# Kernel optimization log

Hardware: AMD Instinct MI355X
Metric: run time of the kernel (lower is better)

Reference implementation:

```python
import jax, jax.numpy as jnp
import numpy as np

B, L, D0, H, K = 16, 256, 64, 128, 512  # batch, seq, feat, hidden, codebook size


def _p(key, shape, scale=0.05):
    return jax.random.normal(key, shape, jnp.float32) * scale


def setup_inputs() -> dict:
    key = jax.random.key(0)
    ks = jax.random.split(key, 32)
    inp = {
        "inputs": jax.random.normal(ks[0], (B, L, D0), jnp.float32),
        "input_lens": jnp.full((B,), L, dtype=jnp.int64),
        "in_mask": jnp.ones((B, L), jnp.float32),
        # encoder params
        "enc_lin1_W": _p(ks[1], (H, D0)), "enc_lin1_b": jnp.zeros((H,), jnp.float32),
        "enc_Wih_f": _p(ks[2], (4 * H, H)), "enc_Whh_f": _p(ks[3], (4 * H, H)), "enc_b_f": jnp.zeros((4 * H,), jnp.float32),
        "enc_Wih_b": _p(ks[4], (4 * H, H)), "enc_Whh_b": _p(ks[5], (4 * H, H)), "enc_b_b": jnp.zeros((4 * H,), jnp.float32),
        "enc_lin2_W": _p(ks[6], (H, 2 * H)), "enc_lin2_b": jnp.zeros((H,), jnp.float32),
        # VQ codebook (K codes of dim H), init uniform(-1/K, 1/K) as in torch
        "vq_emb": jax.random.uniform(ks[7], (K, H), jnp.float32, -1.0 / K, 1.0 / K),
        # decoder params
        "dec_lin1_W": _p(ks[8], (H, D0)), "dec_lin1_b": jnp.zeros((H,), jnp.float32),
        "dec_Wih": _p(ks[9], (4 * H, H)), "dec_Whh": _p(ks[10], (4 * H, H)), "dec_b": jnp.zeros((4 * H,), jnp.float32),
        "attn_Wq": _p(ks[11], (H, H)), "attn_bq": jnp.zeros((H,), jnp.float32),
        "attn_Wk": _p(ks[12], (H, H)), "attn_bk": jnp.zeros((H,), jnp.float32),
        "attn_Wv": _p(ks[13], (H, H)), "attn_bv": jnp.zeros((H,), jnp.float32),
        "dec_lin2_W": _p(ks[14], (D0, H)), "dec_lin2_b": jnp.zeros((D0,), jnp.float32),
    }
    return inp


def _lstm_cell(x, h, c, Wih, Whh, b):
    g = x @ Wih.T + h @ Whh.T + b  # (B, 4H)
    i, f, gg, o = jnp.split(g, 4, axis=-1)
    c = jax.nn.sigmoid(f) * c + jax.nn.sigmoid(i) * jnp.tanh(gg)
    h = jax.nn.sigmoid(o) * jnp.tanh(c)
    return h, c


def _lstm_scan(x_blh, Wih, Whh, b, reverse=False):
    Bb = x_blh.shape[0]
    Hh = Whh.shape[1]
    init = (jnp.zeros((Bb, Hh), x_blh.dtype), jnp.zeros((Bb, Hh), x_blh.dtype))

    def step(carry, x):
        h, c = _lstm_cell(x, carry[0], carry[1], Wih, Whh, b)
        return (h, c), h

    _, hs = jax.lax.scan(step, init, jnp.swapaxes(x_blh, 0, 1), reverse=reverse)
    return jnp.swapaxes(hs, 0, 1)  # (B, L, H)


def _forward(inputs, in_mask, p):
    # ---- encoder: Linear -> ReLU -> BiLSTM -> Linear (full-length sequences) ----
    enc_x = jax.nn.relu(inputs @ p["enc_lin1_W"].T + p["enc_lin1_b"])
    hf = _lstm_scan(enc_x, p["enc_Wih_f"], p["enc_Whh_f"], p["enc_b_f"], reverse=False)
    hb = _lstm_scan(enc_x, p["enc_Wih_b"], p["enc_Whh_b"], p["enc_b_b"], reverse=True)
    ze = jnp.concatenate([hf, hb], axis=-1) @ p["enc_lin2_W"].T + p["enc_lin2_b"]  # (B,L,H)

    # ---- VQ: nearest codebook entry (expanded ||a-b||^2, avoids (B,L,K,C) tensor) ----
    emb = p["vq_emb"]  # (K, H)
    dist = (jnp.sum(ze * ze, -1, keepdims=True)
            - 2.0 * jnp.einsum("blc,kc->blk", ze, emb)
            + jnp.sum(emb * emb, -1)[None, None, :])  # (B,L,K)
    nearest = jnp.argmin(dist, axis=-1)  # (B,L) int
    zq = emb[nearest]  # (B,L,H)
    dec_in = ze + jax.lax.stop_gradient(zq - ze)  # straight-through

    k_proj = dec_in @ p["attn_Wk"].T + p["attn_bk"]  # (B,L,H)
    v_proj = dec_in @ p["attn_Wv"].T + p["attn_bv"]
    scale = 1.0 / jnp.sqrt(jnp.float32(H))
    mask_add = jnp.where(in_mask == 0, -1e9, 0.0).astype(jnp.float32)  # (B,L)

    def dec_step(carry, _):
        h, c, tok = carry
        x = jax.nn.relu(tok @ p["dec_lin1_W"].T + p["dec_lin1_b"])  # (B,H)
        h, c = _lstm_cell(x, h, c, p["dec_Wih"], p["dec_Whh"], p["dec_b"])
        q = h @ p["attn_Wq"].T + p["attn_bq"]  # (B,H)
        scores = jnp.einsum("bd,bld->bl", q, k_proj) * scale + mask_add
        attn = jax.nn.softmax(scores, axis=-1)  # (B,L)
        ctx = jnp.einsum("bl,bld->bd", attn, v_proj)  # (B,H)
        out = ctx @ p["dec_lin2_W"].T + p["dec_lin2_b"]  # (B,D0)
        return (h, c, out), (out, attn)

    Bb = inputs.shape[0]
    init = (jnp.zeros((Bb, H), jnp.float32), jnp.zeros((Bb, H), jnp.float32), jnp.zeros((Bb, D0), jnp.float32))
    _, (outs, attns) = jax.lax.scan(dec_step, init, None, length=dec_in.shape[1])
    dec_out = jnp.swapaxes(outs, 0, 1)  # (B,L,D0)
    attn_w = jnp.swapaxes(attns, 0, 1)  # (B,L,L)
    return dec_out, attn_w, ze, zq


def reference(inputs, input_lens, in_mask, enc_lin1_W, enc_lin1_b, enc_Wih_f, enc_Whh_f, enc_b_f,
              enc_Wih_b, enc_Whh_b, enc_b_b, enc_lin2_W, enc_lin2_b, vq_emb,
              dec_lin1_W, dec_lin1_b, dec_Wih, dec_Whh, dec_b,
              attn_Wq, attn_bq, attn_Wk, attn_bk, attn_Wv, attn_bv, dec_lin2_W, dec_lin2_b):
    p = dict(enc_lin1_W=enc_lin1_W, enc_lin1_b=enc_lin1_b, enc_Wih_f=enc_Wih_f, enc_Whh_f=enc_Whh_f,
             enc_b_f=enc_b_f, enc_Wih_b=enc_Wih_b, enc_Whh_b=enc_Whh_b, enc_b_b=enc_b_b,
             enc_lin2_W=enc_lin2_W, enc_lin2_b=enc_lin2_b, vq_emb=vq_emb,
             dec_lin1_W=dec_lin1_W, dec_lin1_b=dec_lin1_b, dec_Wih=dec_Wih, dec_Whh=dec_Whh, dec_b=dec_b,
             attn_Wq=attn_Wq, attn_bq=attn_bq, attn_Wk=attn_Wk, attn_bk=attn_bk,
             attn_Wv=attn_Wv, attn_bv=attn_bv, dec_lin2_W=dec_lin2_W, dec_lin2_b=dec_lin2_b)
    return _forward(inputs, in_mask, p)
```

## Files before the change

### kernel.cpp

```cpp
#include <hip/hip_runtime.h>

#define Bn  16
#define Ln  256
#define D0n 64
#define Hn  128
#define H4n 512
#define Kn  512
#define BLn 4096

typedef float f4 __attribute__((ext_vector_type(4)));
typedef unsigned long long u64;

__device__ __forceinline__ float sigf(float x) { return 1.0f / (1.0f + expf(-x)); }

__device__ __forceinline__ float fma4v(f4 w, f4 x, float acc) {
    acc = fmaf(w.x, x.x, acc);
    acc = fmaf(w.y, x.y, acc);
    acc = fmaf(w.z, x.z, acc);
    acc = fmaf(w.w, x.w, acc);
    return acc;
}

__device__ __forceinline__ float dotn(const f4* __restrict__ a,
                                      const f4* __restrict__ w, int n4) {
    float a0 = 0.f, a1 = 0.f, a2 = 0.f, a3 = 0.f;
    for (int i = 0; i < n4; i += 4) {
        a0 = fma4v(a[i], w[i], a0);
        a1 = fma4v(a[i + 1], w[i + 1], a1);
        a2 = fma4v(a[i + 2], w[i + 2], a2);
        a3 = fma4v(a[i + 3], w[i + 3], a3);
    }
    return (a0 + a1) + (a2 + a3);
}

__device__ __forceinline__ void tag_store(u64* p, float v, unsigned tag) {
    u64 pk = ((u64)tag << 32) | (u64)__float_as_uint(v);
    __hip_atomic_store(p, pk, __ATOMIC_RELAXED, __HIP_MEMORY_SCOPE_AGENT);
}
__device__ __forceinline__ float tag_poll(u64* p, unsigned tag) {
    u64 v;
    do {
        v = __hip_atomic_load(p, __ATOMIC_RELAXED, __HIP_MEMORY_SCOPE_AGENT);
    } while ((unsigned)(v >> 32) != tag);
    return __uint_as_float((unsigned)v);
}

__global__ __launch_bounds__(256)
void k_gemm(const float* __restrict__ X, const float* __restrict__ W,
            const float* __restrict__ b, float* __restrict__ Y,
            int K, int out_dim, int do_relu, float scale) {
    __shared__ __align__(16) f4 wt4[4096];
    const int K4 = K >> 2;
    const int tid = threadIdx.x;
    const int c = tid & 63, rpart = tid >> 6;
    const f4* W4 = (const f4*)W;
    const int per = K4 >> 2;
    for (int j = 0; j < per; ++j) {
        int col = rpart * per + j;
        wt4[col * 64 + c] = W4[(size_t)(blockIdx.x * 64 + c) * K4 + col];
    }
    __syncthreads();
    const f4* X4 = (const f4*)X;
    const float bc = b ? b[blockIdx.x * 64 + c] : 0.f;
    const int cidx = blockIdx.x * 64 + c;
    for (int i = 0; i < 4; ++i) {
        int rbase = blockIdx.y * 64 + i * 16 + rpart * 4;
        const f4* xr0 = X4 + (size_t)(rbase + 0) * K4;
        const f4* xr1 = X4 + (size_t)(rbase + 1) * K4;
        const f4* xr2 = X4 + (size_t)(rbase + 2) * K4;
        const f4* xr3 = X4 + (size_t)(rbase + 3) * K4;
        float a0 = 0.f, a1 = 0.f, a2 = 0.f, a3 = 0.f;
        for (int k4 = 0; k4 < K4; ++k4) {
            f4 wv = wt4[k4 * 64 + c];
            a0 = fma4v(wv, xr0[k4], a0);
            a1 = fma4v(wv, xr1[k4], a1);
            a2 = fma4v(wv, xr2[k4], a2);
            a3 = fma4v(wv, xr3[k4], a3);
        }
        a0 = scale * a0 + bc; a1 = scale * a1 + bc;
        a2 = scale * a2 + bc; a3 = scale * a3 + bc;
        if (do_relu) {
            a0 = fmaxf(a0, 0.f); a1 = fmaxf(a1, 0.f);
            a2 = fmaxf(a2, 0.f); a3 = fmaxf(a3, 0.f);
        }
        Y[(size_t)(rbase + 0) * out_dim + cidx] = a0;
        Y[(size_t)(rbase + 1) * out_dim + cidx] = a1;
        Y[(size_t)(rbase + 2) * out_dim + cidx] = a2;
        Y[(size_t)(rbase + 3) * out_dim + cidx] = a3;
    }
}

__global__ void k_prep(const float* __restrict__ attn_Wq, float* __restrict__ WqT,
                       const f4* __restrict__ dec_Wih, f4* __restrict__ WihL,
                       const f4* __restrict__ whf, const f4* __restrict__ whb,
                       f4* __restrict__ WhhL, int* __restrict__ zbuf) {
    const int blk = blockIdx.x, tid = threadIdx.x;
    if (blk < 64) {
        int idx = blk * 256 + tid;
        int c = idx >> 7, r = idx & 127;
        WqT[idx] = attn_Wq[(size_t)r * Hn + c];
    } else if (blk < 128) {
        int idx = (blk - 64) * 256 + tid;
        int t = idx & 511, side = (idx >> 9) & 1, k = idx >> 10;
        int rl = t >> 1;
        int grow = (rl >> 6) * 128 + side * 64 + (rl & 63);
        WihL[idx] = dec_Wih[(size_t)grow * 32 + (t & 1) * 16 + k];
    } else if (blk < 192) {
        int idx = (blk - 128) * 256 + tid;
        int row = idx & 511, k = (idx >> 9) & 15, dir = idx >> 13;
        const f4* src = dir ? whb : whf;
        WhhL[idx] = src[(size_t)row * 32 + 16 + k];
    } else {
        int idx = (blk - 192) * 256 + tid;
        if (idx < 8192) zbuf[idx] = 0;
    }
}

__global__ void k_rearrKQF(const f4* __restrict__ in, f4* __restrict__ out) {
    int idx = blockIdx.x * blockDim.x + threadIdx.x;
    if (idx >= 131072) return;
    int tid = idx & 511, k = (idx >> 9) & 15, b = idx >> 13;
    out[idx] = in[((size_t)b * 256 + (tid >> 1)) * 32 + (tid & 1) * 16 + k];
}

__global__ void k_cst(const float* __restrict__ kp, const float* __restrict__ bq,
                      const float* __restrict__ mask, float* __restrict__ cst) {
    int p = blockIdx.x * blockDim.x + threadIdx.x;
    if (p >= BLn) return;
    float a = dotn((const f4*)bq, (const f4*)(kp + (size_t)p * Hn), Hn >> 2);
    cst[p] = a * 0.088388347648318447f + (mask[p] == 0.f ? -1e9f : 0.f);
}

__global__ void k_codenorm(const float* __restrict__ emb, float* __restrict__ c2) {
    int k = blockIdx.x * blockDim.x + threadIdx.x;
    if (k >= Kn) return;
    const f4* e4 = (const f4*)(emb + (size_t)k * Hn);
    float acc = 0.f;
    for (int i = 0; i < Hn / 4; ++i) {
        f4 v = e4[i];
        acc = fmaf(v.x, v.x, acc); acc = fmaf(v.y, v.y, acc);
        acc = fmaf(v.z, v.z, acc); acc = fmaf(v.w, v.w, acc);
    }
    c2[k] = acc;
}

__global__ __launch_bounds__(128)
void k_vqpick(const float* __restrict__ dist, const float* __restrict__ emb,
              float* __restrict__ zq) {
    const int p = blockIdx.x, tid = threadIdx.x;
    __shared__ int best_s;
    if (tid < 64) {
        float best = 3.0e38f; int bi = 0;
        for (int j = 0; j < 8; ++j) {
            int k = j * 64 + tid;
            float d = dist[(size_t)p * Kn + k];
            if (d < best) { best = d; bi = k; }
        }
        for (int off = 32; off > 0; off >>= 1) {
            float ov = __shfl_xor(best, off);
            int   oi = __shfl_xor(bi, off);
            if (ov < best || (ov == best && oi < bi)) { best = ov; bi = oi; }
        }
        if (tid == 0) best_s = bi;
    }
    __syncthreads();
    zq[(size_t)p * Hn + tid] = emb[(size_t)best_s * Hn + tid];
}

__global__ __launch_bounds__(512, 1)
void k_lstm3(const float* __restrict__ xWf, const float* __restrict__ xWb,
             const float* __restrict__ Whh_f, const float* __restrict__ Whh_b,
             const float* __restrict__ WhhL_g, float* __restrict__ hcat) {
    const int b   = blockIdx.x & 15;
    const int dir = blockIdx.x >> 4;
    const int tid = threadIdx.x;
    const float* xW  = dir ? xWb : xWf;
    const f4* Whh4   = (const f4*)(dir ? Whh_b : Whh_f);

    __shared__ __align__(16) f4 wh2_s[16 * 512];
    __shared__ __align__(16) float h_s[Hn];
    __shared__ float g_s[H4n];

    f4 w[16];
#pragma unroll
    for (int f = 0; f < 16; ++f) w[f] = Whh4[(size_t)tid * 32 + f];
#pragma unroll
    for (int f = 0; f < 16; ++f) asm volatile("" : "+v"(w[f]));

    const f4* WhhL4 = (const f4*)WhhL_g;
#pragma unroll
    for (int k = 0; k < 16; ++k)
        wh2_s[k * 512 + tid] = WhhL4[(size_t)dir * 8192 + k * 512 + tid];

    float c_reg = 0.f;
    if (tid < Hn) h_s[tid] = 0.f;

    const int t0 = dir ? (Ln - 1) : 0;
    float xw_v = xW[((size_t)b * Ln + t0) * H4n + tid];
    __syncthreads();

    for (int s = 0; s < Ln; ++s) {
        const int t = dir ? (Ln - 1 - s) : s;
        float xw_n = 0.f;
        if (s + 1 < Ln) {
            int tn = dir ? (Ln - 2 - s) : (s + 1);
            xw_n = xW[((size_t)b * Ln + tn) * H4n + tid];
        }
        {
            const f4* h4 = (const f4*)h_s;
            float a0 = 0.f, a1 = 0.f, a2 = 0.f, a3 = 0.f;
#pragma unroll
            for (int f = 0; f < 16; f += 4) {
                a0 = fma4v(w[f],     h4[f],     a0);
                a1 = fma4v(w[f + 1], h4[f + 1], a1);
                a2 = fma4v(w[f + 2], h4[f + 2], a2);
                a3 = fma4v(w[f + 3], h4[f + 3], a3);
            }
#pragma unroll
            for (int f = 0; f < 16; f += 4) {
                a0 = fma4v(wh2_s[f * 512 + tid],       h4[16 + f],     a0);
                a1 = fma4v(wh2_s[(f + 1) * 512 + tid], h4[16 + f + 1], a1);
                a2 = fma4v(wh2_s[(f + 2) * 512 + tid], h4[16 + f + 2], a2);
                a3 = fma4v(wh2_s[(f + 3) * 512 + tid], h4[16 + f + 3], a3);
            }
            g_s[tid] = (a0 + a1) + (a2 + a3) + xw_v;
        }
        __syncthreads();
        if (tid < Hn) {
            float ig = sigf(g_s[tid]);
            float fg = sigf(g_s[Hn + tid]);
            float gg = tanhf(g_s[2 * Hn + tid]);
            float og = sigf(g_s[3 * Hn + tid]);
            c_reg = fg * c_reg + ig * gg;
            float hv = og * tanhf(c_reg);
            h_s[tid] = hv;
            hcat[((size_t)b * Ln + t) * (2 * Hn) + dir * Hn + tid] = hv;
        }
        __syncthreads();
        xw_v = xw_n;
    }
}

__global__ __launch_bounds__(512, 1)
void k_decoder(const float* __restrict__ kqF_g, const float* __restrict__ vw_g,
               const float* __restrict__ cst_g,
               const float* __restrict__ W1,  const float* __restrict__ b1_g,
               const float* __restrict__ WihL_g, const float* __restrict__ Whh,
               const float* __restrict__ bd_g, u64* gxd,
               float* __restrict__ dec_out, float* __restrict__ attn_w) {
    const int b    = blockIdx.x & 15;
    const int side = blockIdx.x >> 4;
    const int tid  = threadIdx.x;

    __shared__ __align__(16) f4 wih_s[16 * 512];
    __shared__ __align__(16) float tok_s[D0n];
    __shared__ __align__(16) float x_s[Hn];
    __shared__ __align__(16) float h_s[Hn];
    __shared__ float g_loc[256];
    __shared__ float s_s[Ln];
    __shared__ float attn_sp[8][33];
    __shared__ float cst_s[Ln];
    __shared__ float b1_s[Hn];

    const int rl = tid >> 1, ghalf = tid & 1;
    const int grow = (rl >> 6) * 128 + side * 64 + (rl & 63);

    const f4* Whh4 = (const f4*)Whh;
    f4 whh[16];
#pragma unroll
    for (int f = 0; f < 16; ++f) whh[f] = Whh4[(size_t)grow * 32 + ghalf * 16 + f];
    float bdr = bd_g[grow];
    const int o = tid >> 3, slab = tid & 7;
    float vwr[32];
#pragma unroll
    for (int l = 0; l < 32; ++l)
        vwr[l] = vw_g[((size_t)b * Ln + slab * 32 + l) * D0n + o];
#pragma unroll
    for (int f = 0; f < 16; ++f) asm volatile("" : "+v"(whh[f]));
#pragma unroll
    for (int l = 0; l < 32; ++l) asm volatile("" : "+v"(vwr[l]));
    asm volatile("" : "+v"(bdr));

    const f4* WihL4 = (const f4*)WihL_g;
#pragma unroll
    for (int k = 0; k < 16; ++k)
        wih_s[k * 512 + tid] = WihL4[(size_t)k * 1024 + side * 512 + tid];
    if (tid < D0n) tok_s[tid] = 0.f;
    if (tid < Hn)  { h_s[tid] = 0.f; b1_s[tid] = b1_g[tid]; }
    if (tid < Ln)  cst_s[tid] = cst_g[(size_t)b * Ln + tid];
    float c_reg = 0.f;
    __syncthreads();

    u64* gx_mine = gxd + (b * 2 + side) * 128;
    u64* gx_peer = gxd + (b * 2 + (side ^ 1)) * 128;

    const int ar = tid >> 2, ap = tid & 3;
    const f4* W1_4 = (const f4*)W1;
    const f4* kqF  = (const f4*)kqF_g + (size_t)b * 8192;
    const int dbase = (tid & 1) * 16;

    for (int t = 0; t < Ln; ++t) {
        {
            const f4* t4 = (const f4*)tok_s;
            float u0 = 0.f, u1 = 0.f;
#pragma unroll
            for (int k = 0; k < 4; k += 2) {
                f4 wa  = W1_4[(size_t)ar * 16 + ap * 4 + k];
                f4 wb2 = W1_4[(size_t)ar * 16 + ap * 4 + k + 1];
                u0 = fma4v(wa,  t4[ap * 4 + k],     u0);
                u1 = fma4v(wb2, t4[ap * 4 + k + 1], u1);
            }
            float a = u0 + u1;
            a += __shfl_xor(a, 1);
            a += __shfl_xor(a, 2);
            if (ap == 0) x_s[ar] = fmaxf(a + b1_s[ar], 0.f);
        }
        __syncthreads();
        {
            const f4* x4 = (const f4*)x_s + ghalf * 16;
            const f4* h4 = (const f4*)h_s + ghalf * 16;
            float a0 = 0.f, a1 = 0.f, a2 = 0.f, a3 = 0.f;
#pragma unroll
            for (int f = 0; f < 16; f += 4) {
                a0 = fma4v(wih_s[f * 512 + tid],       x4[f],     a0);
                a1 = fma4v(wih_s[(f + 1) * 512 + tid], x4[f + 1], a1);
                a2 = fma4v(wih_s[(f + 2) * 512 + tid], x4[f + 2], a2);
                a3 = fma4v(wih_s[(f + 3) * 512 + tid], x4[f + 3], a3);
            }
#pragma unroll
            for (int f = 0; f < 16; f += 4) {
                a0 = fma4v(whh[f],     h4[f],     a0);
                a1 = fma4v(whh[f + 1], h4[f + 1], a1);
                a2 = fma4v(whh[f + 2], h4[f + 2], a2);
                a3 = fma4v(whh[f + 3], h4[f + 3], a3);
            }
            float a = (a0 + a1) + (a2 + a3);
            a += __shfl_xor(a, 1);
            if (ghalf == 0) g_loc[rl] = a + bdr;
        }
        __syncthreads();
        if (tid < 64) {
            float ig = sigf(g_loc[tid]);
            float fg = sigf(g_loc[64 + tid]);
            float gg = tanhf(g_loc[128 + tid]);
            float og = sigf(g_loc[192 + tid]);
            c_reg = fg * c_reg + ig * gg;
            float hv = og * tanhf(c_reg);
            h_s[side * 64 + tid] = hv;
            tag_store(&gx_mine[(t & 1) * 64 + tid], hv, (unsigned)(t + 1));
            h_s[(side ^ 1) * 64 + tid] =
                tag_poll(&gx_peer[(t & 1) * 64 + tid], (unsigned)(t + 1));
        }
        __syncthreads();
        {
            const f4* h4 = (const f4*)h_s;
            float a0 = 0.f, a1 = 0.f;
#pragma unroll
            for (int k = 0; k < 16; k += 2) {
                f4 q0 = kqF[(size_t)k * 512 + tid];
                f4 q1 = kqF[(size_t)(k + 1) * 512 + tid];
                a0 = fma4v(q0, h4[dbase + k],     a0);
                a1 = fma4v(q1, h4[dbase + k + 1], a1);
            }
            float a = a0 + a1;
            a += __shfl_xor(a, 1);
            if ((tid & 1) == 0) s_s[tid >> 1] = a + cst_s[tid >> 1];
        }
        __syncthreads();
        if (tid < 64) {
            float v0 = s_s[tid],       v1 = s_s[tid + 64];
            float v2 = s_s[tid + 128], v3 = s_s[tid + 192];
            float m = fmaxf(fmaxf(v0, v1), fmaxf(v2, v3));
#pragma unroll
            for (int o2 = 32; o2 > 0; o2 >>= 1) m = fmaxf(m, __shfl_xor(m, o2));
            float e0 = expf(v0 - m), e1 = expf(v1 - m);
            float e2 = expf(v2 - m), e3 = expf(v3 - m);
            float ss = (e0 + e1) + (e2 + e3);
#pragma unroll
            for (int o2 = 32; o2 > 0; o2 >>= 1) ss += __shfl_xor(ss, o2);
            float inv = 1.f / ss;
            e0 *= inv; e1 *= inv; e2 *= inv; e3 *= inv;
            attn_sp[tid >> 5][tid & 31] = e0;
            attn_sp[(tid + 64) >> 5][tid & 31] = e1;
            attn_sp[(tid + 128) >> 5][tid & 31] = e2;
            attn_sp[(tid + 192) >> 5][tid & 31] = e3;
            if (side == 0) {
                float* aw = attn_w + ((size_t)b * Ln + t) * Ln;
                aw[tid] = e0; aw[tid + 64] = e1;
                aw[tid + 128] = e2; aw[tid + 192] = e3;
            }
        }
        __syncthreads();
        {
            const float* as = attn_sp[slab];
            float g0 = 0.f, g1 = 0.f, g2 = 0.f, g3 = 0.f;
#pragma unroll
            for (int l = 0; l < 32; l += 4) {
                g0 = fmaf(as[l],     vwr[l],     g0);
                g1 = fmaf(as[l + 1], vwr[l + 1], g1);
                g2 = fmaf(as[l + 2], vwr[l + 2], g2);
                g3 = fmaf(as[l + 3], vwr[l + 3], g3);
            }
            float a = (g0 + g1) + (g2 + g3);
            a += __shfl_xor(a, 1);
            a += __shfl_xor(a, 2);
            a += __shfl_xor(a, 4);
            if (slab == 0) {
                tok_s[o] = a;
                if (side == 1) dec_out[((size_t)b * Ln + t) * D0n + o] = a;
            }
        }
        __syncthreads();
    }
}

extern "C" void kernel_launch(void* const* d_in, const int* in_sizes, int n_in,
                              void* d_out, int out_size, void* d_ws, size_t ws_size,
                              hipStream_t stream) {
    const float* inputs     = (const float*)d_in[0];
    const float* in_mask    = (const float*)d_in[2];
    const float* enc_lin1_W = (const float*)d_in[3];
    const float* enc_lin1_b = (const float*)d_in[4];
    const float* enc_Wih_f  = (const float*)d_in[5];
    const float* enc_Whh_f  = (const float*)d_in[6];
    const float* enc_b_f    = (const float*)d_in[7];
    const float* enc_Wih_b  = (const float*)d_in[8];
    const float* enc_Whh_b  = (const float*)d_in[9];
    const float* enc_b_b    = (const float*)d_in[10];
    const float* enc_lin2_W = (const float*)d_in[11];
    const float* enc_lin2_b = (const float*)d_in[12];
    const float* vq_emb     = (const float*)d_in[13];
    const float* dec_lin1_W = (const float*)d_in[14];
    const float* dec_lin1_b = (const float*)d_in[15];
    const float* dec_Wih    = (const float*)d_in[16];
    const float* dec_Whh    = (const float*)d_in[17];
    const float* dec_b      = (const float*)d_in[18];
    const float* attn_Wq    = (const float*)d_in[19];
    const float* attn_bq    = (const float*)d_in[20];
    const float* attn_Wk    = (const float*)d_in[21];
    const float* attn_bk    = (const float*)d_in[22];
    const float* attn_Wv    = (const float*)d_in[23];
    const float* attn_bv    = (const float*)d_in[24];
    const float* dec_lin2_W = (const float*)d_in[25];
    const float* dec_lin2_b = (const float*)d_in[26];

    float* out     = (float*)d_out;
    float* dec_out = out;
    float* attn_w  = out + 262144;
    float* ze      = out + 1310720;
    float* zq      = out + 1835008;

    float* ws    = (float*)d_ws;
    float* enc_x = ws;
    float* xWf   = enc_x + 524288;
    float* xWb   = xWf + 2097152;
    float* hcat  = xWb + 2097152;
    float* kp    = hcat + 1048576;
    float* vp    = kp + 524288;
    float* c2    = vp + 524288;
    u64*   gxd   = (u64*)(c2 + 512);
    float* WqT   = enc_x;
    float* WihL  = enc_x + 16384;
    float* WhhL  = enc_x + 16384 + 65536;
    float* dist  = xWf;
    float* KQF   = xWf;
    float* kq    = xWb;
    float* vw    = xWb + 524288;
    float* cst   = xWb + 786432;

    dim3 blk(256);
    k_gemm<<<dim3(2, 64), blk, 0, stream>>>(inputs, enc_lin1_W, enc_lin1_b, enc_x, D0n, Hn, 1, 1.f);
    k_gemm<<<dim3(8, 64), blk, 0, stream>>>(enc_x, enc_Wih_f, enc_b_f, xWf, Hn, H4n, 0, 1.f);
    k_gemm<<<dim3(8, 64), blk, 0, stream>>>(enc_x, enc_Wih_b, enc_b_b, xWb, Hn, H4n, 0, 1.f);
    k_prep<<<224, 256, 0, stream>>>(attn_Wq, WqT, (const f4*)dec_Wih, (f4*)WihL,
                                    (const f4*)enc_Whh_f, (const f4*)enc_Whh_b,
                                    (f4*)WhhL, (int*)gxd);
    k_lstm3<<<32, 512, 0, stream>>>(xWf, xWb, enc_Whh_f, enc_Whh_b, WhhL, hcat);
    k_gemm<<<dim3(2, 64), blk, 0, stream>>>(hcat, enc_lin2_W, enc_lin2_b, ze, 2 * Hn, Hn, 0, 1.f);
    k_codenorm<<<2, 256, 0, stream>>>(vq_emb, c2);
    k_gemm<<<dim3(8, 64), blk, 0, stream>>>(ze, vq_emb, c2, dist, Hn, Kn, 0, -2.f);
    k_vqpick<<<BLn, 128, 0, stream>>>(dist, vq_emb, zq);
    k_gemm<<<dim3(2, 64), blk, 0, stream>>>(zq, attn_Wk, attn_bk, kp, Hn, Hn, 0, 1.f);
    k_gemm<<<dim3(2, 64), blk, 0, stream>>>(zq, attn_Wv, attn_bv, vp, Hn, Hn, 0, 1.f);
    k_gemm<<<dim3(2, 64), blk, 0, stream>>>(kp, WqT, nullptr, kq, Hn, Hn, 0, 0.088388347648318447f);
    k_rearrKQF<<<512, 256, 0, stream>>>((const f4*)kq, (f4*)KQF);
    k_gemm<<<dim3(1, 64), blk, 0, stream>>>(vp, dec_lin2_W, dec_lin2_b, vw, Hn, D0n, 0, 1.f);
    k_cst<<<Bn, 256, 0, stream>>>(kp, attn_bq, in_mask, cst);
    k_decoder<<<32, 512, 0, stream>>>(KQF, vw, cst,
                                      dec_lin1_W, dec_lin1_b,
                                      WihL, dec_Whh, dec_b, gxd,
                                      dec_out, attn_w);
}
```

Baseline: 1.671 ms.

## Fold attention K/Q/V and output projections into precomputed combined weights

Precomputes Wq^T·Wk (scaled) and W2·Wv as combined weight matrices, plus the matching bias terms, inside the prep kernel. A single GEMM from zq then yields both the key-query product and the value-output projection, replacing four GEMMs and the kp/vp intermediates. The two encoder input GEMMs are merged into one launch, and the codebook-norm kernel is folded into prep. This cuts launch count and intermediate traffic, but the weight products are now computed by a naive per-thread loop in prep, and reassociating the products may change rounding slightly.

After: 1.590 ms. 4.8% less time.

```diff
diff --git a/kernel.cpp b/kernel.cpp
--- a/kernel.cpp
+++ b/kernel.cpp
@@ -90,28 +90,127 @@
     }
 }
 
-__global__ void k_prep(const float* __restrict__ attn_Wq, float* __restrict__ WqT,
+__global__ __launch_bounds__(256)
+void k_gemm2(const float* __restrict__ X,
+             const float* __restrict__ Wf, const float* __restrict__ bf,
+             float* __restrict__ Yf,
+             const float* __restrict__ Wb, const float* __restrict__ bb,
+             float* __restrict__ Yb, int K, int out_dim) {
+    __shared__ __align__(16) f4 wt4[4096];
+    const float* W = blockIdx.z ? Wb : Wf;
+    const float* bb_ = blockIdx.z ? bb : bf;
+    float* Y = blockIdx.z ? Yb : Yf;
+    const int K4 = K >> 2;
+    const int tid = threadIdx.x;
+    const int c = tid & 63, rpart = tid >> 6;
+    const f4* W4 = (const f4*)W;
+    const int per = K4 >> 2;
+    for (int j = 0; j < per; ++j) {
+        int col = rpart * per + j;
+        wt4[col * 64 + c] = W4[(size_t)(blockIdx.x * 64 + c) * K4 + col];
+    }
+    __syncthreads();
+    const f4* X4 = (const f4*)X;
+    const float bc = bb_[blockIdx.x * 64 + c];
+    const int cidx = blockIdx.x * 64 + c;
+    for (int i = 0; i < 4; ++i) {
+        int rbase = blockIdx.y * 64 + i * 16 + rpart * 4;
+        const f4* xr0 = X4 + (size_t)(rbase + 0) * K4;
+        const f4* xr1 = X4 + (size_t)(rbase + 1) * K4;
+        const f4* xr2 = X4 + (size_t)(rbase + 2) * K4;
+        const f4* xr3 = X4 + (size_t)(rbase + 3) * K4;
+        float a0 = 0.f, a1 = 0.f, a2 = 0.f, a3 = 0.f;
+        for (int k4 = 0; k4 < K4; ++k4) {
+            f4 wv = wt4[k4 * 64 + c];
+            a0 = fma4v(wv, xr0[k4], a0);
+            a1 = fma4v(wv, xr1[k4], a1);
+            a2 = fma4v(wv, xr2[k4], a2);
+            a3 = fma4v(wv, xr3[k4], a3);
+        }
+        Y[(size_t)(rbase + 0) * out_dim + cidx] = a0 + bc;
+        Y[(size_t)(rbase + 1) * out_dim + cidx] = a1 + bc;
+        Y[(size_t)(rbase + 2) * out_dim + cidx] = a2 + bc;
+        Y[(size_t)(rbase + 3) * out_dim + cidx] = a3 + bc;
+    }
+}
+
+#define SCL 0.088388347648318447f
+
+__global__ void k_prep(const float* __restrict__ Wq, const float* __restrict__ Wk,
+                       const float* __restrict__ Wv, const float* __restrict__ W2,
+                       const float* __restrict__ bk, const float* __restrict__ bv,
+                       const float* __restrict__ b2, const float* __restrict__ bq,
+                       float* __restrict__ Wcat, float* __restrict__ bcat,
+                       float* __restrict__ u, float* __restrict__ ub,
                        const f4* __restrict__ dec_Wih, f4* __restrict__ WihL,
                        const f4* __restrict__ whf, const f4* __restrict__ whb,
-                       f4* __restrict__ WhhL, int* __restrict__ zbuf) {
+                       f4* __restrict__ WhhL,
+                       const float* __restrict__ emb, float* __restrict__ c2,
+                       int* __restrict__ zbuf) {
     const int blk = blockIdx.x, tid = threadIdx.x;
     if (blk < 64) {
         int idx = blk * 256 + tid;
-        int c = idx >> 7, r = idx & 127;
-        WqT[idx] = attn_Wq[(size_t)r * Hn + c];
-    } else if (blk < 128) {
+        int c = idx >> 7, d = idx & 127;
+        float acc = 0.f;
+        for (int r = 0; r < Hn; ++r)
+            acc = fmaf(Wq[(size_t)r * Hn + c], Wk[(size_t)r * Hn + d], acc);
+        Wcat[(size_t)c * Hn + d] = SCL * acc;
+    } else if (blk < 96) {
         int idx = (blk - 64) * 256 + tid;
+        int o = idx >> 7, d = idx & 127;
+        float acc = 0.f;
+        for (int r = 0; r < Hn; ++r)
+            acc = fmaf(W2[(size_t)o * Hn + r], Wv[(size_t)r * Hn + d], acc);
+        Wcat[(size_t)(128 + o) * Hn + d] = acc;
+    } else if (blk < 160) {
+        int idx = (blk - 96) * 256 + tid;
         int t = idx & 511, side = (idx >> 9) & 1, k = idx >> 10;
         int rl = t >> 1;
         int grow = (rl >> 6) * 128 + side * 64 + (rl & 63);
         WihL[idx] = dec_Wih[(size_t)grow * 32 + (t & 1) * 16 + k];
-    } else if (blk < 192) {
-        int idx = (blk - 128) * 256 + tid;
+    } else if (blk < 224) {
+        int idx = (blk - 160) * 256 + tid;
         int row = idx & 511, k = (idx >> 9) & 15, dir = idx >> 13;
         const f4* src = dir ? whb : whf;
         WhhL[idx] = src[(size_t)row * 32 + 16 + k];
+    } else if (blk == 224) {
+        if (tid < 128) {
+            float acc = 0.f;
+            for (int r = 0; r < Hn; ++r)
+                acc = fmaf(Wq[(size_t)r * Hn + tid], bk[r], acc);
+            bcat[tid] = SCL * acc;
+        } else if (tid < 192) {
+            int o = tid - 128;
+            float acc = b2[o];
+            for (int r = 0; r < Hn; ++r)
+                acc = fmaf(W2[(size_t)o * Hn + r], bv[r], acc);
+            bcat[tid] = acc;
+        }
+    } else if (blk == 225) {
+        if (tid < 128) {
+            float acc = 0.f;
+            for (int r = 0; r < Hn; ++r)
+                acc = fmaf(bq[r], Wk[(size_t)r * Hn + tid], acc);
+            u[tid] = SCL * acc;
+        } else if (tid == 128) {
+            float acc = 0.f;
+            for (int r = 0; r < Hn; ++r) acc = fmaf(bq[r], bk[r], acc);
+            ub[0] = SCL * acc;
+        }
+    } else if (blk < 228) {
+        int k = (blk - 226) * 256 + tid;
+        if (k < Kn) {
+            const f4* e4 = (const f4*)(emb + (size_t)k * Hn);
+            float acc = 0.f;
+            for (int i = 0; i < Hn / 4; ++i) {
+                f4 v = e4[i];
+                acc = fmaf(v.x, v.x, acc); acc = fmaf(v.y, v.y, acc);
+                acc = fmaf(v.z, v.z, acc); acc = fmaf(v.w, v.w, acc);
+            }
+            c2[k] = acc;
+        }
     } else {
-        int idx = (blk - 192) * 256 + tid;
+        int idx = (blk - 228) * 256 + tid;
         if (idx < 8192) zbuf[idx] = 0;
     }
 }
@@ -120,28 +219,16 @@
     int idx = blockIdx.x * blockDim.x + threadIdx.x;
     if (idx >= 131072) return;
     int tid = idx & 511, k = (idx >> 9) & 15, b = idx >> 13;
-    out[idx] = in[((size_t)b * 256 + (tid >> 1)) * 32 + (tid & 1) * 16 + k];
-}
-
-__global__ void k_cst(const float* __restrict__ kp, const float* __restrict__ bq,
-                      const float* __restrict__ mask, float* __restrict__ cst) {
+    out[idx] = in[((size_t)b * 256 + (tid >> 1)) * 48 + (tid & 1) * 16 + k];
+}
+
+__global__ void k_cst(const float* __restrict__ zq, const float* __restrict__ u,
+                      const float* __restrict__ ub, const float* __restrict__ mask,
+                      float* __restrict__ cst) {
     int p = blockIdx.x * blockDim.x + threadIdx.x;
     if (p >= BLn) return;
-    float a = dotn((const f4*)bq, (const f4*)(kp + (size_t)p * Hn), Hn >> 2);
-    cst[p] = a * 0.088388347648318447f + (mask[p] == 0.f ? -1e9f : 0.f);
-}
-
-__global__ void k_codenorm(const float* __restrict__ emb, float* __restrict__ c2) {
-    int k = blockIdx.x * blockDim.x + threadIdx.x;
-    if (k >= Kn) return;
-    const f4* e4 = (const f4*)(emb + (size_t)k * Hn);
-    float acc = 0.f;
-    for (int i = 0; i < Hn / 4; ++i) {
-        f4 v = e4[i];
-        acc = fmaf(v.x, v.x, acc); acc = fmaf(v.y, v.y, acc);
-        acc = fmaf(v.z, v.z, acc); acc = fmaf(v.w, v.w, acc);
-    }
-    c2[k] = acc;
+    float a = dotn((const f4*)u, (const f4*)(zq + (size_t)p * Hn), Hn >> 2);
+    cst[p] = a + ub[0] + (mask[p] == 0.f ? -1e9f : 0.f);
 }
 
 __global__ __launch_bounds__(128)
@@ -242,7 +329,7 @@
 }
 
 __global__ __launch_bounds__(512, 1)
-void k_decoder(const float* __restrict__ kqF_g, const float* __restrict__ vw_g,
+void k_decoder(const float* __restrict__ kqF_g, const float* __restrict__ ycat_g,
                const float* __restrict__ cst_g,
                const float* __restrict__ W1,  const float* __restrict__ b1_g,
                const float* __restrict__ WihL_g, const float* __restrict__ Whh,
@@ -274,7 +361,7 @@
     float vwr[32];
 #pragma unroll
     for (int l = 0; l < 32; ++l)
-        vwr[l] = vw_g[((size_t)b * Ln + slab * 32 + l) * D0n + o];
+        vwr[l] = ycat_g[((size_t)b * Ln + slab * 32 + l) * 192 + 128 + o];
 #pragma unroll
     for (int f = 0; f < 16; ++f) asm volatile("" : "+v"(whh[f]));
 #pragma unroll
@@ -455,38 +542,39 @@
     float* xWf   = enc_x + 524288;
     float* xWb   = xWf + 2097152;
     float* hcat  = xWb + 2097152;
-    float* kp    = hcat + 1048576;
-    float* vp    = kp + 524288;
-    float* c2    = vp + 524288;
-    u64*   gxd   = (u64*)(c2 + 512);
-    float* WqT   = enc_x;
-    float* WihL  = enc_x + 16384;
-    float* WhhL  = enc_x + 16384 + 65536;
+    float* base2 = hcat + 1048576;
+    float* c2    = base2;
+    u64*   gxd   = (u64*)(base2 + 512);
+    float* Wcat  = base2 + 512 + 8192;
+    float* bcat  = Wcat + 24576;
+    float* uvec  = bcat + 256;
+    float* ubv   = uvec + 128;
+    float* WihL  = ubv + 16;
+    float* WhhL  = WihL + 65536;
     float* dist  = xWf;
     float* KQF   = xWf;
-    float* kq    = xWb;
-    float* vw    = xWb + 524288;
+    float* Ycat  = xWb;
     float* cst   = xWb + 786432;
 
     dim3 blk(256);
+    k_prep<<<260, 256, 0, stream>>>(attn_Wq, attn_Wk, attn_Wv, dec_lin2_W,
+                                    attn_bk, attn_bv, dec_lin2_b, attn_bq,
+                                    Wcat, bcat, uvec, ubv,
+                                    (const f4*)dec_Wih, (f4*)WihL,
+                                    (const f4*)enc_Whh_f, (const f4*)enc_Whh_b,
+                                    (f4*)WhhL, vq_emb, c2, (int*)gxd);
     k_gemm<<<dim3(2, 64), blk, 0, stream>>>(inputs, enc_lin1_W, enc_lin1_b, enc_x, D0n, Hn, 1, 1.f);
-    k_gemm<<<dim3(8, 64), blk, 0, stream>>>(enc_x, enc_Wih_f, enc_b_f, xWf, Hn, H4n, 0, 1.f);
-    k_gemm<<<dim3(8, 64), blk, 0, stream>>>(enc_x, enc_Wih_b, enc_b_b, xWb, Hn, H4n, 0, 1.f);
-    k_prep<<<224, 256, 0, stream>>>(attn_Wq, WqT, (const f4*)dec_Wih, (f4*)WihL,
-                                    (const f4*)enc_Whh_f, (const f4*)enc_Whh_b,
-                                    (f4*)WhhL, (int*)gxd);
+    k_gemm2<<<dim3(8, 64, 2), blk, 0, stream>>>(enc_x,
+                                                enc_Wih_f, enc_b_f, xWf,
+                                                enc_Wih_b, enc_b_b, xWb, Hn, H4n);
     k_lstm3<<<32, 512, 0, stream>>>(xWf, xWb, enc_Whh_f, enc_Whh_b, WhhL, hcat);
     k_gemm<<<dim3(2, 64), blk, 0, stream>>>(hcat, enc_lin2_W, enc_lin2_b, ze, 2 * Hn, Hn, 0, 1.f);
-    k_codenorm<<<2, 256, 0, stream>>>(vq_emb, c2);
     k_gemm<<<dim3(8, 64), blk, 0, stream>>>(ze, vq_emb, c2, dist, Hn, Kn, 0, -2.f);
     k_vqpick<<<BLn, 128, 0, stream>>>(dist, vq_emb, zq);
-    k_gemm<<<dim3(2, 64), blk, 0, stream>>>(zq, attn_Wk, attn_bk, kp, Hn, Hn, 0, 1.f);
-    k_gemm<<<dim3(2, 64), blk, 0, stream>>>(zq, attn_Wv, attn_bv, vp, Hn, Hn, 0, 1.f);
-    k_gemm<<<dim3(2, 64), blk, 0, stream>>>(kp, WqT, nullptr, kq, Hn, Hn, 0, 0.088388347648318447f);
-    k_rearrKQF<<<512, 256, 0, stream>>>((const f4*)kq, (f4*)KQF);
-    k_gemm<<<dim3(1, 64), blk, 0, stream>>>(vp, dec_lin2_W, dec_lin2_b, vw, Hn, D0n, 0, 1.f);
-    k_cst<<<Bn, 256, 0, stream>>>(kp, attn_bq, in_mask, cst);
-    k_decoder<<<32, 512, 0, stream>>>(KQF, vw, cst,
+    k_gemm<<<dim3(3, 64), blk, 0, stream>>>(zq, Wcat, bcat, Ycat, Hn, 192, 0, 1.f);
+    k_cst<<<Bn, 256, 0, stream>>>(zq, uvec, ubv, in_mask, cst);
+    k_rearrKQF<<<512, 256, 0, stream>>>((const f4*)Ycat, (f4*)KQF);
+    k_decoder<<<32, 512, 0, stream>>>(KQF, Ycat, cst,
                                       dec_lin1_W, dec_lin1_b,
                                       WihL, dec_Whh, dec_b, gxd,
                                       dec_out, attn_w);
```
